# Kernel optimization log

Hardware: AMD Instinct MI355X
Metric: run time of the kernel (lower is better)

The kernel has to match this reference:

```python
import jax, jax.numpy as jnp
import numpy as np

N, E = 50000, 800000
IN, MID, OUT = 128, 256, 128
LN_EPS = 1e-5


def layer_norm(x, gamma, beta, eps=LN_EPS):
    mu = jnp.mean(x, axis=-1, keepdims=True)
    var = jnp.mean(jnp.square(x - mu), axis=-1, keepdims=True)
    return (x - mu) * jax.lax.rsqrt(var + eps) * gamma + beta


def gcn_conv(x, W, b, src, dst, norm, n):
    # x' = D^{-1/2}(A+I)D^{-1/2} X W + b  (self-loops already folded into src/dst/norm)
    h = x @ W                                  # [N, F_out]
    msg = h[src] * norm[:, None]               # [E+N, F_out] gather + scale
    out = jax.ops.segment_sum(msg, dst, num_segments=n)
    return out + b


def setup_inputs() -> dict:
    key = jax.random.key(0)
    ks = jax.random.split(key, 4)
    x = jax.random.normal(ks[0], (N, IN), dtype=jnp.float32)
    edge_index = jax.random.randint(ks[1], (2, E), 0, N, dtype=jnp.int32)
    W1 = jax.random.normal(ks[2], (IN, MID), dtype=jnp.float32) * (1.0 / np.sqrt(IN))
    b1 = jnp.zeros((MID,), jnp.float32)
    g1 = jnp.ones((IN,), jnp.float32)
    be1 = jnp.zeros((IN,), jnp.float32)
    W4 = jax.random.normal(ks[3], (MID, OUT), dtype=jnp.float32) * (1.0 / np.sqrt(MID))
    b4 = jnp.zeros((OUT,), jnp.float32)
    g4 = jnp.ones((MID,), jnp.float32)
    be4 = jnp.zeros((MID,), jnp.float32)
    return {"x": x, "W1": W1, "b1": b1, "g1": g1, "be1": be1,
            "W4": W4, "b4": b4, "g4": g4, "be4": be4,
            "edge_index": edge_index}


def reference(x, W1, b1, g1, be1, W4, b4, g4, be4, edge_index):
    n = x.shape[0]
    loop = jnp.arange(n, dtype=edge_index.dtype)
    src = jnp.concatenate([edge_index[0], loop])   # [E+N]
    dst = jnp.concatenate([edge_index[1], loop])   # [E+N]
    deg = jax.ops.segment_sum(jnp.ones_like(src, x.dtype), dst, num_segments=n)
    dinv = jax.lax.rsqrt(deg)                      # deg >= 1 thanks to self-loops
    norm = dinv[src] * dinv[dst]                   # [E+N]

    h = gcn_conv(layer_norm(x, g1, be1), W1, b1, src, dst, norm, n)
    h = jax.nn.gelu(h, approximate=False)          # torch F.gelu default = exact erf
    h = gcn_conv(layer_norm(h, g4, be4), W4, b4, src, dst, norm, n)
    return h
```

## Files before the change

### kernel.cpp

```cpp
#include <hip/hip_runtime.h>
#include <math.h>

#define N_NODES 50000
#define E_EDGES 800000

typedef __attribute__((ext_vector_type(4))) float f32x4;
typedef __attribute__((ext_vector_type(8))) short s16x8;

#define T1_OFF    0UL
#define A1H_OFF   12800000UL
#define A1L_OFF   25600000UL
#define T2B_OFF   38400000UL
#define WB1H_OFF  64000000UL
#define WB1L_OFF  64100096UL
#define WB4H_OFF  64200192UL
#define WB4L_OFF  64300288UL
#define DINV_OFF  64400384UL
#define HIST8_OFF 64600384UL
#define RP8_OFF   66200384UL
#define POSREL_OFF 67800448UL
#define CSRS_OFF  71000448UL
#define BSUM_OFF  74200448UL

__device__ __forceinline__ float lo16f(unsigned u) { return __uint_as_float(u << 16); }
__device__ __forceinline__ float hi16f(unsigned u) { return __uint_as_float(u & 0xffff0000u); }
__device__ __forceinline__ unsigned pack2bf(float a, float b) {
  unsigned ua = __float_as_uint(a); ua += 0x7fffu + ((ua >> 16) & 1u);
  unsigned ub = __float_as_uint(b); ub += 0x7fffu + ((ub >> 16) & 1u);
  return (ua >> 16) | (ub & 0xffff0000u);
}
__device__ __forceinline__ float gelu_f(float x) {
  return 0.5f * x * (1.f + erff(x * 0.70710678118654752f));
}

__device__ __forceinline__ void convW_body(const float* __restrict__ W,
                                           unsigned* __restrict__ Wh,
                                           unsigned* __restrict__ Wl,
                                           int K, int N, int tid) {
  if (tid >= (K * N) / 8) return;
  int c15 = tid & 15;
  int kg  = (tid >> 4) & 3;
  int KS  = K >> 5;
  int ks  = (tid >> 6) % KS;
  int nt  = (tid >> 6) / KS;
  int col = nt * 16 + c15;
  int k0  = ks * 32 + kg * 8;
  float w[8];
  #pragma unroll
  for (int j = 0; j < 8; ++j) w[j] = W[(size_t)(k0 + j) * N + col];
  uint4 h, l;
  h.x = pack2bf(w[0], w[1]); l.x = pack2bf(w[0] - lo16f(h.x), w[1] - hi16f(h.x));
  h.y = pack2bf(w[2], w[3]); l.y = pack2bf(w[2] - lo16f(h.y), w[3] - hi16f(h.y));
  h.z = pack2bf(w[4], w[5]); l.z = pack2bf(w[4] - lo16f(h.z), w[5] - hi16f(h.z));
  h.w = pack2bf(w[6], w[7]); l.w = pack2bf(w[6] - lo16f(h.w), w[7] - hi16f(h.w));
  *reinterpret_cast<uint4*>(Wh + (size_t)tid * 4) = h;
  *reinterpret_cast<uint4*>(Wl + (size_t)tid * 4) = l;
}

__global__ __launch_bounds__(256) void prep_kernel(const float* __restrict__ x,
                                                   const float* __restrict__ g,
                                                   const float* __restrict__ be,
                                                   unsigned* __restrict__ T,
                                                   const float* __restrict__ W1,
                                                   const float* __restrict__ W4,
                                                   unsigned* __restrict__ Wh1,
                                                   unsigned* __restrict__ Wl1,
                                                   unsigned* __restrict__ Wh4,
                                                   unsigned* __restrict__ Wl4,
                                                   int4* __restrict__ hist8v) {
  int b = blockIdx.x;
  if (b < 12500) {
    int lane = threadIdx.x & 63, wv = threadIdx.x >> 6;
    int row = b * 4 + wv;
    float2 v = *reinterpret_cast<const float2*>(x + (size_t)row * 128 + lane * 2);
    float s = v.x + v.y, sq = v.x * v.x + v.y * v.y;
    #pragma unroll
    for (int m = 1; m < 64; m <<= 1) { s += __shfl_xor(s, m); sq += __shfl_xor(sq, m); }
    float mu = s * (1.f / 128.f);
    float var = sq * (1.f / 128.f) - mu * mu;
    float rs = rsqrtf(var + 1e-5f);
    float2 gg = *reinterpret_cast<const float2*>(g + lane * 2);
    float2 bb = *reinterpret_cast<const float2*>(be + lane * 2);
    T[(size_t)row * 64 + lane] =
        pack2bf((v.x - mu) * rs * gg.x + bb.x, (v.y - mu) * rs * gg.y + bb.y);
  } else if (b < 12891) {
    int i = (b - 12500) * 256 + threadIdx.x;
    if (i < 100000) hist8v[i] = make_int4(0, 0, 0, 0);
  } else {
    int bb = b - 12891;
    if (bb < 16) convW_body(W1, Wh1, Wl1, 128, 256, bb * 256 + threadIdx.x);
    else         convW_body(W4, Wh4, Wl4, 256, 128, (bb - 16) * 256 + threadIdx.x);
  }
}

__global__ __launch_bounds__(256) void edge_pos(const int* __restrict__ dst,
                                                int* __restrict__ hist8,
                                                unsigned short* __restrict__ posrel) {
  int t4 = blockIdx.x * 256 + threadIdx.x;
  if (t4 >= E_EDGES / 4) return;
  int e = t4 * 4;
  int seg = blockIdx.x & 7;
  int4 d = *reinterpret_cast<const int4*>(dst + e);
  unsigned long long r = 0;
  r |= (unsigned long long)(unsigned short)atomicAdd(&hist8[d.x * 8 + seg], 1);
  r |= (unsigned long long)(unsigned short)atomicAdd(&hist8[d.y * 8 + seg], 1) << 16;
  r |= (unsigned long long)(unsigned short)atomicAdd(&hist8[d.z * 8 + seg], 1) << 32;
  r |= (unsigned long long)(unsigned short)atomicAdd(&hist8[d.w * 8 + seg], 1) << 48;
  __builtin_nontemporal_store(r, reinterpret_cast<unsigned long long*>(posrel + e));
}

__global__ __launch_bounds__(1024) void scan_partial(const int* __restrict__ hist,
                                                     int* __restrict__ rp,
                                                     int* __restrict__ bsum,
                                                     float* __restrict__ dinv, int n) {
  __shared__ int wsum[16];
  int tid = threadIdx.x, lane = tid & 63, wv = tid >> 6;
  int i = blockIdx.x * 1024 + tid;
  int v = (i < n) ? hist[i] : 0;
  int s8 = v;
  #pragma unroll
  for (int m = 1; m < 8; m <<= 1) s8 += __shfl_xor(s8, m);
  if ((i & 7) == 0 && i < n) dinv[i >> 3] = rsqrtf((float)(s8 + 1));
  int sc = v;
  #pragma unroll
  for (int m = 1; m < 64; m <<= 1) { int o = __shfl_up(sc, m); if (lane >= m) sc += o; }
  if (lane == 63) wsum[wv] = sc;
  __syncthreads();
  if (wv == 0) {
    int w = (lane < 16) ? wsum[lane] : 0;
    int swc = w;
    #pragma unroll
    for (int m = 1; m < 16; m <<= 1) { int o = __shfl_up(swc, m); if (lane >= m) swc += o; }
    if (lane < 16) wsum[lane] = swc - w;
    if (lane == 15) bsum[blockIdx.x] = swc;
  }
  __syncthreads();
  if (i < n) rp[i] = (sc - v) + wsum[wv];
}

__global__ __launch_bounds__(64) void scan_bsums(int* __restrict__ bsum, int nb) {
  int lane = threadIdx.x;
  int carry = 0;
  for (int base = 0; base < nb; base += 64) {
    int i = base + lane;
    int v = (i < nb) ? bsum[i] : 0;
    int sc = v;
    #pragma unroll
    for (int m = 1; m < 64; m <<= 1) { int o = __shfl_up(sc, m); if (lane >= m) sc += o; }
    if (i < nb) bsum[i] = carry + sc - v;
    carry += __shfl(sc, 63);
  }
  if (lane == 0) bsum[nb] = carry;
}

__global__ __launch_bounds__(1024) void scan_add(int* __restrict__ rp,
                                                 const int* __restrict__ bsum, int n) {
  int i = blockIdx.x * 1024 + threadIdx.x;
  if (i < n) rp[i] += bsum[blockIdx.x];
  if (i == 0) rp[n] = bsum[gridDim.x];
}

__global__ __launch_bounds__(256) void fill2(const int* __restrict__ src,
                                             const int* __restrict__ dst,
                                             const int* __restrict__ rp8,
                                             const unsigned short* __restrict__ posrel,
                                             unsigned short* __restrict__ csr_src) {
  int t4 = blockIdx.x * 256 + threadIdx.x;
  if (t4 >= E_EDGES / 4) return;
  int e = t4 * 4;
  int seg = blockIdx.x & 7;
  int4 s = *reinterpret_cast<const int4*>(src + e);
  int4 d = *reinterpret_cast<const int4*>(dst + e);
  unsigned long long pr =
      *reinterpret_cast<const unsigned long long*>(posrel + e);
  __builtin_nontemporal_store((unsigned short)s.x,
      csr_src + rp8[d.x * 8 + seg] + (int)(pr & 0xffff));
  __builtin_nontemporal_store((unsigned short)s.y,
      csr_src + rp8[d.y * 8 + seg] + (int)((pr >> 16) & 0xffff));
  __builtin_nontemporal_store((unsigned short)s.z,
      csr_src + rp8[d.z * 8 + seg] + (int)((pr >> 32) & 0xffff));
  __builtin_nontemporal_store((unsigned short)s.w,
      csr_src + rp8[d.w * 8 + seg] + (int)((pr >> 48) & 0xffff));
}

template <int MODE>
__global__ __launch_bounds__(256) void agg128(const unsigned* __restrict__ T,
                                              const int* __restrict__ rp8,
                                              const unsigned short* __restrict__ csr,
                                              const float* __restrict__ dinv,
                                              const float* __restrict__ b,
                                              float* __restrict__ out,
                                              unsigned* __restrict__ outh,
                                              unsigned* __restrict__ outl) {
  int lane = threadIdx.x & 63, wv = threadIdx.x >> 6;
  int node = blockIdx.x * 4 + wv;
  float di = dinv[node], sn = di * di;
  unsigned us = T[(size_t)node * 64 + lane];
  float a0 = lo16f(us) * sn, a1 = hi16f(us) * sn;
  float b0 = 0.f, b1 = 0.f;
  int e = rp8[node * 8], e1 = rp8[node * 8 + 8];
  if (e + 7 < e1) {
    int sA[8];
    #pragma unroll
    for (int j = 0; j < 8; ++j) sA[j] = csr[e + j];
    for (;;) {
      unsigned u[8];
      float nn[8];
      #pragma unroll
      for (int j = 0; j < 8; ++j) u[j] = T[(size_t)sA[j] * 64 + lane];
      #pragma unroll
      for (int j = 0; j < 8; ++j) nn[j] = dinv[sA[j]];
      e += 8;
      bool more = (e + 7 < e1);
      int sB[8];
      if (more) {
        #pragma unroll
        for (int j = 0; j < 8; ++j) sB[j] = csr[e + j];
      }
      #pragma unroll
      for (int j = 0; j < 8; ++j) {
        float nr = nn[j] * di;
        if (j & 1) { b0 += lo16f(u[j]) * nr; b1 += hi16f(u[j]) * nr; }
        else       { a0 += lo16f(u[j]) * nr; a1 += hi16f(u[j]) * nr; }
      }
      if (!more) break;
      #pragma unroll
      for (int j = 0; j < 8; ++j) sA[j] = sB[j];
    }
  }
  for (; e < e1; ++e) {
    int s = csr[e];
    unsigned u = T[(size_t)s * 64 + lane];
    float nr = dinv[s] * di;
    a0 += lo16f(u) * nr; a1 += hi16f(u) * nr;
  }
  a0 += b0; a1 += b1;
  if (MODE == 0) {
    unsigned h = pack2bf(a0, a1);
    float r0 = a0 - lo16f(h), r1 = a1 - hi16f(h);
    outh[(size_t)node * 64 + lane] = h;
    outl[(size_t)node * 64 + lane] = pack2bf(r0, r1);
  } else {
    float2 bb = *reinterpret_cast<const float2*>(b + lane * 2);
    *reinterpret_cast<float2*>(out + (size_t)node * 128 + lane * 2) =
        make_float2(a0 + bb.x, a1 + bb.y);
  }
}

__global__ __launch_bounds__(256) void gemm1_fused(const unsigned* __restrict__ Ah,
                                                   const unsigned* __restrict__ Al,
                                                   const unsigned* __restrict__ Wh,
                                                   const unsigned* __restrict__ Wl,
                                                   const float* __restrict__ b,
                                                   const float* __restrict__ g,
                                                   const float* __restrict__ be,
                                                   unsigned* __restrict__ T2b, int n) {
  __shared__ float st[32 * 260];
  int t = threadIdx.x, lane = t & 63, w = t >> 6;
  int kg = lane >> 4, c15 = lane & 15;
  int c0 = w * 64;
  int row0 = blockIdx.x * 32 + c15;
  int r0 = min(row0, n - 1);
  int r1 = min(row0 + 16, n - 1);
  const unsigned* ah0 = Ah + (size_t)r0 * 64 + kg * 4;
  const unsigned* al0 = Al + (size_t)r0 * 64 + kg * 4;
  const unsigned* ah1 = Ah + (size_t)r1 * 64 + kg * 4;
  const unsigned* al1 = Al + (size_t)r1 * 64 + kg * 4;
  f32x4 acc[2][4];
  #pragma unroll
  for (int rt = 0; rt < 2; ++rt)
    #pragma unroll
    for (int nf = 0; nf < 4; ++nf) acc[rt][nf] = (f32x4)(0.f);
  #pragma unroll
  for (int ks = 0; ks < 4; ++ks) {
    s16x8 bh[4], bl[4];
    #pragma unroll
    for (int nf = 0; nf < 4; ++nf) {
      int nt = (c0 >> 4) + nf;
      size_t bo = (size_t)(((nt * 4 + ks) * 4 + kg) * 16 + c15) * 4;
      bh[nf] = *reinterpret_cast<const s16x8*>(Wh + bo);
      bl[nf] = *reinterpret_cast<const s16x8*>(Wl + bo);
    }
    s16x8 a0h = *reinterpret_cast<const s16x8*>(ah0 + ks * 16);
    s16x8 a0l = *reinterpret_cast<const s16x8*>(al0 + ks * 16);
    s16x8 a1h = *reinterpret_cast<const s16x8*>(ah1 + ks * 16);
    s16x8 a1l = *reinterpret_cast<const s16x8*>(al1 + ks * 16);
    #pragma unroll
    for (int nf = 0; nf < 4; ++nf) {
      acc[0][nf] = __builtin_amdgcn_mfma_f32_16x16x32_bf16(a0h, bh[nf], acc[0][nf], 0, 0, 0);
      acc[0][nf] = __builtin_amdgcn_mfma_f32_16x16x32_bf16(a0l, bh[nf], acc[0][nf], 0, 0, 0);
      acc[0][nf] = __builtin_amdgcn_mfma_f32_16x16x32_bf16(a0h, bl[nf], acc[0][nf], 0, 0, 0);
      acc[1][nf] = __builtin_amdgcn_mfma_f32_16x16x32_bf16(a1h, bh[nf], acc[1][nf], 0, 0, 0);
      acc[1][nf] = __builtin_amdgcn_mfma_f32_16x16x32_bf16(a1l, bh[nf], acc[1][nf], 0, 0, 0);
      acc[1][nf] = __builtin_amdgcn_mfma_f32_16x16x32_bf16(a1h, bl[nf], acc[1][nf], 0, 0, 0);
    }
  }
  #pragma unroll
  for (int rt = 0; rt < 2; ++rt)
    #pragma unroll
    for (int nf = 0; nf < 4; ++nf) {
      int col = c0 + nf * 16 + c15;
      float bb = b[col];
      #pragma unroll
      for (int r = 0; r < 4; ++r) {
        int row = rt * 16 + kg * 4 + r;
        st[row * 260 + col] = gelu_f(acc[rt][nf][r] + bb);
      }
    }
  __syncthreads();
  float4 gg = *reinterpret_cast<const float4*>(g + lane * 4);
  float4 bb2 = *reinterpret_cast<const float4*>(be + lane * 4);
  #pragma unroll
  for (int rr = 0; rr < 8; ++rr) {
    int row = w * 8 + rr;
    float4 v = *reinterpret_cast<const float4*>(&st[row * 260 + lane * 4]);
    float s = v.x + v.y + v.z + v.w;
    float sq = v.x * v.x + v.y * v.y + v.z * v.z + v.w * v.w;
    #pragma unroll
    for (int m = 1; m < 64; m <<= 1) { s += __shfl_xor(s, m); sq += __shfl_xor(sq, m); }
    float mu = s * (1.f / 256.f);
    float var = sq * (1.f / 256.f) - mu * mu;
    float rs = rsqrtf(var + 1e-5f);
    int gr = blockIdx.x * 32 + row;
    if (gr < n) {
      uint2 p;
      p.x = pack2bf((v.x - mu) * rs * gg.x + bb2.x, (v.y - mu) * rs * gg.y + bb2.y);
      p.y = pack2bf((v.z - mu) * rs * gg.z + bb2.z, (v.w - mu) * rs * gg.w + bb2.w);
      *reinterpret_cast<uint2*>(T2b + (size_t)gr * 128 + lane * 2) = p;
    }
  }
}

__global__ __launch_bounds__(256) void gemm2_mfma(const unsigned* __restrict__ Ab,
                                                  const unsigned* __restrict__ Wh,
                                                  const unsigned* __restrict__ Wl,
                                                  unsigned* __restrict__ T2, int n) {
  __shared__ float st[32 * 132];
  int t = threadIdx.x, lane = t & 63, w = t >> 6;
  int kg = lane >> 4, c15 = lane & 15;
  int c0 = w * 32;
  int row0 = blockIdx.x * 32 + c15;
  int r0 = min(row0, n - 1);
  int r1 = min(row0 + 16, n - 1);
  const unsigned* ap0 = Ab + (size_t)r0 * 128 + kg * 4;
  const unsigned* ap1 = Ab + (size_t)r1 * 128 + kg * 4;
  f32x4 acc[2][2];
  #pragma unroll
  for (int rt = 0; rt < 2; ++rt) { acc[rt][0] = (f32x4)(0.f); acc[rt][1] = (f32x4)(0.f); }
  #pragma unroll
  for (int ks = 0; ks < 8; ++ks) {
    s16x8 bh[2], bl[2];
    #pragma unroll
    for (int nf = 0; nf < 2; ++nf) {
      int nt = (c0 >> 4) + nf;
      size_t bo = (size_t)(((nt * 8 + ks) * 4 + kg) * 16 + c15) * 4;
      bh[nf] = *reinterpret_cast<const s16x8*>(Wh + bo);
      bl[nf] = *reinterpret_cast<const s16x8*>(Wl + bo);
    }
    s16x8 a0 = *reinterpret_cast<const s16x8*>(ap0 + ks * 16);
    s16x8 a1 = *reinterpret_cast<const s16x8*>(ap1 + ks * 16);
    #pragma unroll
    for (int nf = 0; nf < 2; ++nf) {
      acc[0][nf] = __builtin_amdgcn_mfma_f32_16x16x32_bf16(a0, bh[nf], acc[0][nf], 0, 0, 0);
      acc[0][nf] = __builtin_amdgcn_mfma_f32_16x16x32_bf16(a0, bl[nf], acc[0][nf], 0, 0, 0);
      acc[1][nf] = __builtin_amdgcn_mfma_f32_16x16x32_bf16(a1, bh[nf], acc[1][nf], 0, 0, 0);
      acc[1][nf] = __builtin_amdgcn_mfma_f32_16x16x32_bf16(a1, bl[nf], acc[1][nf], 0, 0, 0);
    }
  }
  #pragma unroll
  for (int rt = 0; rt < 2; ++rt)
    #pragma unroll
    for (int nf = 0; nf < 2; ++nf) {
      int col = c0 + nf * 16 + c15;
      #pragma unroll
      for (int r = 0; r < 4; ++r) {
        int row = rt * 16 + kg * 4 + r;
        st[row * 132 + col] = acc[rt][nf][r];
      }
    }
  __syncthreads();
  #pragma unroll
  for (int rr = 0; rr < 8; ++rr) {
    int row = w * 8 + rr;
    int gr = blockIdx.x * 32 + row;
    if (gr < n) {
      float2 v = *reinterpret_cast<const float2*>(&st[row * 132 + lane * 2]);
      T2[(size_t)gr * 64 + lane] = pack2bf(v.x, v.y);
    }
  }
}

extern "C" void kernel_launch(void* const* d_in, const int* in_sizes, int n_in,
                              void* d_out, int out_size, void* d_ws, size_t ws_size,
                              hipStream_t stream) {
  (void)in_sizes; (void)n_in; (void)out_size; (void)ws_size;
  const float* x   = (const float*)d_in[0];
  const float* W1  = (const float*)d_in[1];
  const float* b1  = (const float*)d_in[2];
  const float* g1  = (const float*)d_in[3];
  const float* be1 = (const float*)d_in[4];
  const float* W4  = (const float*)d_in[5];
  const float* b4  = (const float*)d_in[6];
  const float* g4  = (const float*)d_in[7];
  const float* be4 = (const float*)d_in[8];
  const int*   ei  = (const int*)d_in[9];
  const int* src = ei;
  const int* dst = ei + E_EDGES;

  char* ws = (char*)d_ws;
  unsigned* T1    = (unsigned*)(ws + T1_OFF);
  unsigned* T2    = (unsigned*)(ws + T1_OFF);
  unsigned* A1h   = (unsigned*)(ws + A1H_OFF);
  unsigned* A1l   = (unsigned*)(ws + A1L_OFF);
  unsigned* T2b   = (unsigned*)(ws + T2B_OFF);
  unsigned* Wb1h  = (unsigned*)(ws + WB1H_OFF);
  unsigned* Wb1l  = (unsigned*)(ws + WB1L_OFF);
  unsigned* Wb4h  = (unsigned*)(ws + WB4H_OFF);
  unsigned* Wb4l  = (unsigned*)(ws + WB4L_OFF);
  float* dinv     = (float*)(ws + DINV_OFF);
  int*   hist8    = (int*)(ws + HIST8_OFF);
  int*   rp8      = (int*)(ws + RP8_OFF);
  unsigned short* posrel  = (unsigned short*)(ws + POSREL_OFF);
  unsigned short* csr_src = (unsigned short*)(ws + CSRS_OFF);
  int*   bsum     = (int*)(ws + BSUM_OFF);
  float* outp     = (float*)d_out;

  const int NSEG = N_NODES * 8;
  int nblkE4 = (E_EDGES / 4 + 255) / 256;
  int nbScan = (NSEG + 1023) / 1024;
  int nblkG  = (N_NODES + 31) / 32;
  int nblkP  = 12500 + 391 + 32;

  hipLaunchKernelGGL(prep_kernel, dim3(nblkP), dim3(256), 0, stream,
                     x, g1, be1, T1, W1, W4, Wb1h, Wb1l, Wb4h, Wb4l, (int4*)hist8);
  hipLaunchKernelGGL(edge_pos, dim3(nblkE4), dim3(256), 0, stream, dst, hist8, posrel);
  hipLaunchKernelGGL(scan_partial, dim3(nbScan), dim3(1024), 0, stream,
                     hist8, rp8, bsum, dinv, NSEG);
  hipLaunchKernelGGL(scan_bsums, dim3(1), dim3(64), 0, stream, bsum, nbScan);
  hipLaunchKernelGGL(scan_add, dim3(nbScan), dim3(1024), 0, stream, rp8, bsum, NSEG);
  hipLaunchKernelGGL(fill2, dim3(nblkE4), dim3(256), 0, stream, src, dst, rp8, posrel, csr_src);

  hipLaunchKernelGGL(agg128<0>, dim3(N_NODES / 4), dim3(256), 0, stream,
                     T1, rp8, csr_src, dinv, (const float*)nullptr,
                     (float*)nullptr, A1h, A1l);
  hipLaunchKernelGGL(gemm1_fused, dim3(nblkG), dim3(256), 0, stream,
                     A1h, A1l, Wb1h, Wb1l, b1, g4, be4, T2b, N_NODES);

  hipLaunchKernelGGL(gemm2_mfma, dim3(nblkG), dim3(256), 0, stream, T2b, Wb4h, Wb4l, T2, N_NODES);
  hipLaunchKernelGGL(agg128<2>, dim3(N_NODES / 4), dim3(256), 0, stream,
                     T2, rp8, csr_src, dinv, b4, outp,
                     (unsigned*)nullptr, (unsigned*)nullptr);
}
```

Before: 230.7 us.

## Chunk feature tables into 32-column slabs and precompute fp16 edge norms in CSR

Feature tables T1/T2 are stored as four column chunks (16 dwords per node each), so each aggregation block handles one chunk for a group of nodes. The goal is a smaller per-chunk working set that stays in cache during the random gathers. The CSR entries now pack the source index with a precomputed fp16 normalization, removing the per-edge dinv gathers. Each wavefront processes four edges in parallel and reduces across quarter-wavefronts with shuffles. The cost is eight times as many aggregation blocks, a 32-bit CSR that is twice the size, and fp16 rounding of the norm coefficients.

New measurement: 271.2 us. 1.18x slower.

```diff
diff --git a/kernel.cpp b/kernel.cpp
--- a/kernel.cpp
+++ b/kernel.cpp
@@ -1,8 +1,10 @@
 #include <hip/hip_runtime.h>
+#include <hip/hip_fp16.h>
 #include <math.h>
 
 #define N_NODES 50000
 #define E_EDGES 800000
+#define CHUNK_U (N_NODES * 16)
 
 typedef __attribute__((ext_vector_type(4))) float f32x4;
 typedef __attribute__((ext_vector_type(8))) short s16x8;
@@ -19,7 +21,7 @@
 #define HIST8_OFF 64600384UL
 #define RP8_OFF   66200384UL
 #define POSREL_OFF 67800448UL
-#define CSRS_OFF  71000448UL
+#define CSR_OFF   71000448UL
 #define BSUM_OFF  74200448UL
 
 __device__ __forceinline__ float lo16f(unsigned u) { return __uint_as_float(u << 16); }
@@ -31,6 +33,14 @@
 }
 __device__ __forceinline__ float gelu_f(float x) {
   return 0.5f * x * (1.f + erff(x * 0.70710678118654752f));
+}
+__device__ __forceinline__ unsigned short f2h_bits(float f) {
+  __half h = __float2half_rn(f);
+  return *reinterpret_cast<unsigned short*>(&h);
+}
+__device__ __forceinline__ float h_bits2f(unsigned short u) {
+  __half h = *reinterpret_cast<__half*>(&u);
+  return __half2float(h);
 }
 
 __device__ __forceinline__ void convW_body(const float* __restrict__ W,
@@ -81,7 +91,7 @@
     float rs = rsqrtf(var + 1e-5f);
     float2 gg = *reinterpret_cast<const float2*>(g + lane * 2);
     float2 bb = *reinterpret_cast<const float2*>(be + lane * 2);
-    T[(size_t)row * 64 + lane] =
+    T[(size_t)(lane >> 4) * CHUNK_U + (size_t)row * 16 + (lane & 15)] =
         pack2bf((v.x - mu) * rs * gg.x + bb.x, (v.y - mu) * rs * gg.y + bb.y);
   } else if (b < 12891) {
     int i = (b - 12500) * 256 + threadIdx.x;
@@ -164,86 +174,91 @@
                                              const int* __restrict__ dst,
                                              const int* __restrict__ rp8,
                                              const unsigned short* __restrict__ posrel,
-                                             unsigned short* __restrict__ csr_src) {
+                                             const float* __restrict__ dinv,
+                                             unsigned* __restrict__ csr) {
   int t4 = blockIdx.x * 256 + threadIdx.x;
   if (t4 >= E_EDGES / 4) return;
   int e = t4 * 4;
   int seg = blockIdx.x & 7;
   int4 s = *reinterpret_cast<const int4*>(src + e);
   int4 d = *reinterpret_cast<const int4*>(dst + e);
-  unsigned long long pr =
-      *reinterpret_cast<const unsigned long long*>(posrel + e);
-  __builtin_nontemporal_store((unsigned short)s.x,
-      csr_src + rp8[d.x * 8 + seg] + (int)(pr & 0xffff));
-  __builtin_nontemporal_store((unsigned short)s.y,
-      csr_src + rp8[d.y * 8 + seg] + (int)((pr >> 16) & 0xffff));
-  __builtin_nontemporal_store((unsigned short)s.z,
-      csr_src + rp8[d.z * 8 + seg] + (int)((pr >> 32) & 0xffff));
-  __builtin_nontemporal_store((unsigned short)s.w,
-      csr_src + rp8[d.w * 8 + seg] + (int)((pr >> 48) & 0xffff));
+  unsigned long long pr = *reinterpret_cast<const unsigned long long*>(posrel + e);
+  int ss[4] = {s.x, s.y, s.z, s.w};
+  int dd[4] = {d.x, d.y, d.z, d.w};
+  #pragma unroll
+  for (int j = 0; j < 4; ++j) {
+    int pos = rp8[dd[j] * 8 + seg] + (int)((pr >> (16 * j)) & 0xffff);
+    float nr = dinv[ss[j]] * dinv[dd[j]];
+    unsigned pk = ((unsigned)f2h_bits(nr) << 16) | (unsigned)ss[j];
+    __builtin_nontemporal_store(pk, csr + pos);
+  }
 }
 
 template <int MODE>
-__global__ __launch_bounds__(256) void agg128(const unsigned* __restrict__ T,
-                                              const int* __restrict__ rp8,
-                                              const unsigned short* __restrict__ csr,
-                                              const float* __restrict__ dinv,
-                                              const float* __restrict__ b,
-                                              float* __restrict__ out,
-                                              unsigned* __restrict__ outh,
-                                              unsigned* __restrict__ outl) {
-  int lane = threadIdx.x & 63, wv = threadIdx.x >> 6;
-  int node = blockIdx.x * 4 + wv;
-  float di = dinv[node], sn = di * di;
-  unsigned us = T[(size_t)node * 64 + lane];
-  float a0 = lo16f(us) * sn, a1 = hi16f(us) * sn;
+__global__ __launch_bounds__(256) void agg32(const unsigned* __restrict__ Tc,
+                                             const int* __restrict__ rp8,
+                                             const unsigned* __restrict__ csr,
+                                             const float* __restrict__ dinv,
+                                             const float* __restrict__ b,
+                                             float* __restrict__ out,
+                                             unsigned* __restrict__ outh,
+                                             unsigned* __restrict__ outl) {
+  int t = threadIdx.x, lane = t & 63, wv = t >> 6;
+  int bid = blockIdx.x;
+  int cid = bid & 7;
+  int chunk = cid >> 1, half = cid & 1;
+  int node = (bid >> 3) * 8 + half * 4 + wv;
+  int q = lane >> 4, l16 = lane & 15;
+  const unsigned* Tch = Tc + (size_t)chunk * CHUNK_U;
+  float a0 = 0.f, a1 = 0.f;
   float b0 = 0.f, b1 = 0.f;
-  int e = rp8[node * 8], e1 = rp8[node * 8 + 8];
-  if (e + 7 < e1) {
-    int sA[8];
-    #pragma unroll
-    for (int j = 0; j < 8; ++j) sA[j] = csr[e + j];
-    for (;;) {
-      unsigned u[8];
-      float nn[8];
-      #pragma unroll
-      for (int j = 0; j < 8; ++j) u[j] = T[(size_t)sA[j] * 64 + lane];
-      #pragma unroll
-      for (int j = 0; j < 8; ++j) nn[j] = dinv[sA[j]];
-      e += 8;
-      bool more = (e + 7 < e1);
-      int sB[8];
-      if (more) {
-        #pragma unroll
-        for (int j = 0; j < 8; ++j) sB[j] = csr[e + j];
-      }
-      #pragma unroll
-      for (int j = 0; j < 8; ++j) {
-        float nr = nn[j] * di;
-        if (j & 1) { b0 += lo16f(u[j]) * nr; b1 += hi16f(u[j]) * nr; }
-        else       { a0 += lo16f(u[j]) * nr; a1 += hi16f(u[j]) * nr; }
-      }
-      if (!more) break;
-      #pragma unroll
-      for (int j = 0; j < 8; ++j) sA[j] = sB[j];
-    }
-  }
-  for (; e < e1; ++e) {
-    int s = csr[e];
-    unsigned u = T[(size_t)s * 64 + lane];
-    float nr = dinv[s] * di;
-    a0 += lo16f(u) * nr; a1 += hi16f(u) * nr;
+  int e0 = rp8[node * 8], e1 = rp8[node * 8 + 8];
+  int e = e0;
+  for (; e + 16 <= e1; e += 16) {
+    unsigned c0 = csr[e + q];
+    unsigned c1 = csr[e + 4 + q];
+    unsigned c2 = csr[e + 8 + q];
+    unsigned c3 = csr[e + 12 + q];
+    unsigned u0 = Tch[(size_t)(c0 & 0xffffu) * 16 + l16];
+    unsigned u1 = Tch[(size_t)(c1 & 0xffffu) * 16 + l16];
+    unsigned u2 = Tch[(size_t)(c2 & 0xffffu) * 16 + l16];
+    unsigned u3 = Tch[(size_t)(c3 & 0xffffu) * 16 + l16];
+    float n0 = h_bits2f((unsigned short)(c0 >> 16));
+    float n1 = h_bits2f((unsigned short)(c1 >> 16));
+    float n2 = h_bits2f((unsigned short)(c2 >> 16));
+    float n3 = h_bits2f((unsigned short)(c3 >> 16));
+    a0 += lo16f(u0) * n0; a1 += hi16f(u0) * n0;
+    b0 += lo16f(u1) * n1; b1 += hi16f(u1) * n1;
+    a0 += lo16f(u2) * n2; a1 += hi16f(u2) * n2;
+    b0 += lo16f(u3) * n3; b1 += hi16f(u3) * n3;
+  }
+  if (e < e1) {
+    #pragma unroll
+    for (int j = 0; j < 4; ++j) {
+      int idx = e + j * 4 + q;
+      bool valid = idx < e1;
+      unsigned c = csr[valid ? idx : e0];
+      unsigned u = Tch[(size_t)(c & 0xffffu) * 16 + l16];
+      float nr = valid ? h_bits2f((unsigned short)(c >> 16)) : 0.f;
+      a0 += lo16f(u) * nr; a1 += hi16f(u) * nr;
+    }
   }
   a0 += b0; a1 += b1;
-  if (MODE == 0) {
-    unsigned h = pack2bf(a0, a1);
-    float r0 = a0 - lo16f(h), r1 = a1 - hi16f(h);
-    outh[(size_t)node * 64 + lane] = h;
-    outl[(size_t)node * 64 + lane] = pack2bf(r0, r1);
-  } else {
-    float2 bb = *reinterpret_cast<const float2*>(b + lane * 2);
-    *reinterpret_cast<float2*>(out + (size_t)node * 128 + lane * 2) =
-        make_float2(a0 + bb.x, a1 + bb.y);
+  a0 += __shfl_xor(a0, 16); a1 += __shfl_xor(a1, 16);
+  a0 += __shfl_xor(a0, 32); a1 += __shfl_xor(a1, 32);
+  if (q == 0) {
+    float di = dinv[node], sn = di * di;
+    unsigned us = Tch[(size_t)node * 16 + l16];
+    a0 += lo16f(us) * sn; a1 += hi16f(us) * sn;
+    if (MODE == 0) {
+      unsigned h = pack2bf(a0, a1);
+      outh[(size_t)node * 64 + chunk * 16 + l16] = h;
+      outl[(size_t)node * 64 + chunk * 16 + l16] = pack2bf(a0 - lo16f(h), a1 - hi16f(h));
+    } else {
+      float2 bb = *reinterpret_cast<const float2*>(b + chunk * 32 + l16 * 2);
+      *reinterpret_cast<float2*>(out + (size_t)node * 128 + chunk * 32 + l16 * 2) =
+          make_float2(a0 + bb.x, a1 + bb.y);
+    }
   }
 }
 
@@ -385,7 +400,7 @@
     int gr = blockIdx.x * 32 + row;
     if (gr < n) {
       float2 v = *reinterpret_cast<const float2*>(&st[row * 132 + lane * 2]);
-      T2[(size_t)gr * 64 + lane] = pack2bf(v.x, v.y);
+      T2[(size_t)(lane >> 4) * CHUNK_U + (size_t)gr * 16 + (lane & 15)] = pack2bf(v.x, v.y);
     }
   }
 }
@@ -420,8 +435,8 @@
   float* dinv     = (float*)(ws + DINV_OFF);
   int*   hist8    = (int*)(ws + HIST8_OFF);
   int*   rp8      = (int*)(ws + RP8_OFF);
-  unsigned short* posrel  = (unsigned short*)(ws + POSREL_OFF);
-  unsigned short* csr_src = (unsigned short*)(ws + CSRS_OFF);
+  unsigned short* posrel = (unsigned short*)(ws + POSREL_OFF);
+  unsigned* csr   = (unsigned*)(ws + CSR_OFF);
   int*   bsum     = (int*)(ws + BSUM_OFF);
   float* outp     = (float*)d_out;
 
@@ -430,6 +445,7 @@
   int nbScan = (NSEG + 1023) / 1024;
   int nblkG  = (N_NODES + 31) / 32;
   int nblkP  = 12500 + 391 + 32;
+  int nblkA  = (N_NODES / 8) * 8;
 
   hipLaunchKernelGGL(prep_kernel, dim3(nblkP), dim3(256), 0, stream,
                      x, g1, be1, T1, W1, W4, Wb1h, Wb1l, Wb4h, Wb4l, (int4*)hist8);
@@ -438,16 +454,17 @@
                      hist8, rp8, bsum, dinv, NSEG);
   hipLaunchKernelGGL(scan_bsums, dim3(1), dim3(64), 0, stream, bsum, nbScan);
   hipLaunchKernelGGL(scan_add, dim3(nbScan), dim3(1024), 0, stream, rp8, bsum, NSEG);
-  hipLaunchKernelGGL(fill2, dim3(nblkE4), dim3(256), 0, stream, src, dst, rp8, posrel, csr_src);
-
-  hipLaunchKernelGGL(agg128<0>, dim3(N_NODES / 4), dim3(256), 0, stream,
-                     T1, rp8, csr_src, dinv, (const float*)nullptr,
+  hipLaunchKernelGGL(fill2, dim3(nblkE4), dim3(256), 0, stream,
+                     src, dst, rp8, posrel, dinv, csr);
+
+  hipLaunchKernelGGL(agg32<0>, dim3(nblkA), dim3(256), 0, stream,
+                     T1, rp8, csr, dinv, (const float*)nullptr,
                      (float*)nullptr, A1h, A1l);
   hipLaunchKernelGGL(gemm1_fused, dim3(nblkG), dim3(256), 0, stream,
                      A1h, A1l, Wb1h, Wb1l, b1, g4, be4, T2b, N_NODES);
 
   hipLaunchKernelGGL(gemm2_mfma, dim3(nblkG), dim3(256), 0, stream, T2b, Wb4h, Wb4l, T2, N_NODES);
-  hipLaunchKernelGGL(agg128<2>, dim3(N_NODES / 4), dim3(256), 0, stream,
-                     T2, rp8, csr_src, dinv, b4, outp,
+  hipLaunchKernelGGL(agg32<2>, dim3(nblkA), dim3(256), 0, stream,
+                     T2, rp8, csr, dinv, b4, outp,
                      (unsigned*)nullptr, (unsigned*)nullptr);
 }
```

## Fuse layer-1 aggregation into GEMM1 kernel via shared-memory tiles

Applied to the files above, without the earlier changes.

Merges the first-layer neighbour aggregation with the following GEMM+bias+GELU+LayerNorm kernel. Each block aggregates its 32 nodes into LDS as bf16 hi/lo splits and feeds MFMA directly, so the 128-wide A1 hi/lo intermediates no longer round-trip through global memory and one launch disappears. The LayerNorm epilogue also changes from an LDS-staged full row to register-resident values with a cross-wave reduction through small LDS arrays, then writes bf16 per element. The cost is that each block now serialises 8 node aggregations per wave before its GEMM, and the grid has far fewer blocks, which may reduce latency hiding for the gather-bound part.

After: 268.0 us. 1.16x slower.

```diff
diff --git a/kernel.cpp b/kernel.cpp
--- a/kernel.cpp
+++ b/kernel.cpp
@@ -8,8 +8,6 @@
 typedef __attribute__((ext_vector_type(8))) short s16x8;
 
 #define T1_OFF    0UL
-#define A1H_OFF   12800000UL
-#define A1L_OFF   25600000UL
 #define T2B_OFF   38400000UL
 #define WB1H_OFF  64000000UL
 #define WB1L_OFF  64100096UL
@@ -28,6 +26,10 @@
   unsigned ua = __float_as_uint(a); ua += 0x7fffu + ((ua >> 16) & 1u);
   unsigned ub = __float_as_uint(b); ub += 0x7fffu + ((ub >> 16) & 1u);
   return (ua >> 16) | (ub & 0xffff0000u);
+}
+__device__ __forceinline__ unsigned short bf16r(float f) {
+  unsigned ua = __float_as_uint(f); ua += 0x7fffu + ((ua >> 16) & 1u);
+  return (unsigned short)(ua >> 16);
 }
 __device__ __forceinline__ float gelu_f(float x) {
   return 0.5f * x * (1.f + erff(x * 0.70710678118654752f));
@@ -171,8 +173,7 @@
   int seg = blockIdx.x & 7;
   int4 s = *reinterpret_cast<const int4*>(src + e);
   int4 d = *reinterpret_cast<const int4*>(dst + e);
-  unsigned long long pr =
-      *reinterpret_cast<const unsigned long long*>(posrel + e);
+  unsigned long long pr = *reinterpret_cast<const unsigned long long*>(posrel + e);
   __builtin_nontemporal_store((unsigned short)s.x,
       csr_src + rp8[d.x * 8 + seg] + (int)(pr & 0xffff));
   __builtin_nontemporal_store((unsigned short)s.y,
@@ -183,89 +184,77 @@
       csr_src + rp8[d.w * 8 + seg] + (int)((pr >> 48) & 0xffff));
 }
 
-template <int MODE>
-__global__ __launch_bounds__(256) void agg128(const unsigned* __restrict__ T,
-                                              const int* __restrict__ rp8,
-                                              const unsigned short* __restrict__ csr,
-                                              const float* __restrict__ dinv,
-                                              const float* __restrict__ b,
-                                              float* __restrict__ out,
-                                              unsigned* __restrict__ outh,
-                                              unsigned* __restrict__ outl) {
-  int lane = threadIdx.x & 63, wv = threadIdx.x >> 6;
-  int node = blockIdx.x * 4 + wv;
-  float di = dinv[node], sn = di * di;
-  unsigned us = T[(size_t)node * 64 + lane];
-  float a0 = lo16f(us) * sn, a1 = hi16f(us) * sn;
-  float b0 = 0.f, b1 = 0.f;
-  int e = rp8[node * 8], e1 = rp8[node * 8 + 8];
-  if (e + 7 < e1) {
-    int sA[8];
-    #pragma unroll
-    for (int j = 0; j < 8; ++j) sA[j] = csr[e + j];
-    for (;;) {
-      unsigned u[8];
-      float nn[8];
-      #pragma unroll
-      for (int j = 0; j < 8; ++j) u[j] = T[(size_t)sA[j] * 64 + lane];
-      #pragma unroll
-      for (int j = 0; j < 8; ++j) nn[j] = dinv[sA[j]];
-      e += 8;
-      bool more = (e + 7 < e1);
-      int sB[8];
-      if (more) {
+__global__ __launch_bounds__(256) void layer1_fused(
+    const unsigned* __restrict__ T,
+    const int* __restrict__ rp8,
+    const unsigned short* __restrict__ csr,
+    const float* __restrict__ dinv,
+    const unsigned* __restrict__ Wh,
+    const unsigned* __restrict__ Wl,
+    const float* __restrict__ b,
+    const float* __restrict__ g,
+    const float* __restrict__ be,
+    unsigned short* __restrict__ T2b,
+    int n) {
+  __shared__ unsigned AhL[32][68];
+  __shared__ unsigned AlL[32][68];
+  __shared__ float rsum[32][4];
+  __shared__ float rsq[32][4];
+  int t = threadIdx.x, lane = t & 63, w = t >> 6;
+
+  for (int i = 0; i < 8; ++i) {
+    int nl = w * 8 + i;
+    int node = blockIdx.x * 32 + nl;
+    if (node >= n) node = n - 1;
+    float di = dinv[node], sn = di * di;
+    unsigned us = T[(size_t)node * 64 + lane];
+    float a0 = lo16f(us) * sn, a1 = hi16f(us) * sn;
+    float b0 = 0.f, b1_ = 0.f;
+    int e = rp8[node * 8], e1 = rp8[node * 8 + 8];
+    if (e + 7 < e1) {
+      int sA[8];
+      #pragma unroll
+      for (int j = 0; j < 8; ++j) sA[j] = csr[e + j];
+      for (;;) {
+        unsigned u[8];
+        float nn[8];
         #pragma unroll
-        for (int j = 0; j < 8; ++j) sB[j] = csr[e + j];
+        for (int j = 0; j < 8; ++j) u[j] = T[(size_t)sA[j] * 64 + lane];
+        #pragma unroll
+        for (int j = 0; j < 8; ++j) nn[j] = dinv[sA[j]];
+        e += 8;
+        bool more = (e + 7 < e1);
+        int sB[8];
+        if (more) {
+          #pragma unroll
+          for (int j = 0; j < 8; ++j) sB[j] = csr[e + j];
+        }
+        #pragma unroll
+        for (int j = 0; j < 8; ++j) {
+          float nr = nn[j] * di;
+          if (j & 1) { b0 += lo16f(u[j]) * nr; b1_ += hi16f(u[j]) * nr; }
+          else       { a0 += lo16f(u[j]) * nr; a1 += hi16f(u[j]) * nr; }
+        }
+        if (!more) break;
+        #pragma unroll
+        for (int j = 0; j < 8; ++j) sA[j] = sB[j];
       }
-      #pragma unroll
-      for (int j = 0; j < 8; ++j) {
-        float nr = nn[j] * di;
-        if (j & 1) { b0 += lo16f(u[j]) * nr; b1 += hi16f(u[j]) * nr; }
-        else       { a0 += lo16f(u[j]) * nr; a1 += hi16f(u[j]) * nr; }
-      }
-      if (!more) break;
-      #pragma unroll
-      for (int j = 0; j < 8; ++j) sA[j] = sB[j];
-    }
-  }
-  for (; e < e1; ++e) {
-    int s = csr[e];
-    unsigned u = T[(size_t)s * 64 + lane];
-    float nr = dinv[s] * di;
-    a0 += lo16f(u) * nr; a1 += hi16f(u) * nr;
-  }
-  a0 += b0; a1 += b1;
-  if (MODE == 0) {
+    }
+    for (; e < e1; ++e) {
+      int s = csr[e];
+      unsigned u = T[(size_t)s * 64 + lane];
+      float nr = dinv[s] * di;
+      a0 += lo16f(u) * nr; a1 += hi16f(u) * nr;
+    }
+    a0 += b0; a1 += b1_;
     unsigned h = pack2bf(a0, a1);
-    float r0 = a0 - lo16f(h), r1 = a1 - hi16f(h);
-    outh[(size_t)node * 64 + lane] = h;
-    outl[(size_t)node * 64 + lane] = pack2bf(r0, r1);
-  } else {
-    float2 bb = *reinterpret_cast<const float2*>(b + lane * 2);
-    *reinterpret_cast<float2*>(out + (size_t)node * 128 + lane * 2) =
-        make_float2(a0 + bb.x, a1 + bb.y);
-  }
-}
-
-__global__ __launch_bounds__(256) void gemm1_fused(const unsigned* __restrict__ Ah,
-                                                   const unsigned* __restrict__ Al,
-                                                   const unsigned* __restrict__ Wh,
-                                                   const unsigned* __restrict__ Wl,
-                                                   const float* __restrict__ b,
-                                                   const float* __restrict__ g,
-                                                   const float* __restrict__ be,
-                                                   unsigned* __restrict__ T2b, int n) {
-  __shared__ float st[32 * 260];
-  int t = threadIdx.x, lane = t & 63, w = t >> 6;
+    AhL[nl][lane] = h;
+    AlL[nl][lane] = pack2bf(a0 - lo16f(h), a1 - hi16f(h));
+  }
+  __syncthreads();
+
   int kg = lane >> 4, c15 = lane & 15;
   int c0 = w * 64;
-  int row0 = blockIdx.x * 32 + c15;
-  int r0 = min(row0, n - 1);
-  int r1 = min(row0 + 16, n - 1);
-  const unsigned* ah0 = Ah + (size_t)r0 * 64 + kg * 4;
-  const unsigned* al0 = Al + (size_t)r0 * 64 + kg * 4;
-  const unsigned* ah1 = Ah + (size_t)r1 * 64 + kg * 4;
-  const unsigned* al1 = Al + (size_t)r1 * 64 + kg * 4;
   f32x4 acc[2][4];
   #pragma unroll
   for (int rt = 0; rt < 2; ++rt)
@@ -281,10 +270,10 @@
       bh[nf] = *reinterpret_cast<const s16x8*>(Wh + bo);
       bl[nf] = *reinterpret_cast<const s16x8*>(Wl + bo);
     }
-    s16x8 a0h = *reinterpret_cast<const s16x8*>(ah0 + ks * 16);
-    s16x8 a0l = *reinterpret_cast<const s16x8*>(al0 + ks * 16);
-    s16x8 a1h = *reinterpret_cast<const s16x8*>(ah1 + ks * 16);
-    s16x8 a1l = *reinterpret_cast<const s16x8*>(al1 + ks * 16);
+    s16x8 a0h = *reinterpret_cast<const s16x8*>(&AhL[c15][kg * 4 + ks * 16]);
+    s16x8 a0l = *reinterpret_cast<const s16x8*>(&AlL[c15][kg * 4 + ks * 16]);
+    s16x8 a1h = *reinterpret_cast<const s16x8*>(&AhL[16 + c15][kg * 4 + ks * 16]);
+    s16x8 a1l = *reinterpret_cast<const s16x8*>(&AlL[16 + c15][kg * 4 + ks * 16]);
     #pragma unroll
     for (int nf = 0; nf < 4; ++nf) {
       acc[0][nf] = __builtin_amdgcn_mfma_f32_16x16x32_bf16(a0h, bh[nf], acc[0][nf], 0, 0, 0);
@@ -295,40 +284,57 @@
       acc[1][nf] = __builtin_amdgcn_mfma_f32_16x16x32_bf16(a1h, bl[nf], acc[1][nf], 0, 0, 0);
     }
   }
+
+  float hv[2][4][4];
+  float bb[4], gg[4], be2[4];
+  #pragma unroll
+  for (int nf = 0; nf < 4; ++nf) {
+    int col = c0 + nf * 16 + c15;
+    bb[nf] = b[col]; gg[nf] = g[col]; be2[nf] = be[col];
+  }
   #pragma unroll
   for (int rt = 0; rt < 2; ++rt)
     #pragma unroll
-    for (int nf = 0; nf < 4; ++nf) {
-      int col = c0 + nf * 16 + c15;
-      float bb = b[col];
-      #pragma unroll
-      for (int r = 0; r < 4; ++r) {
+    for (int nf = 0; nf < 4; ++nf)
+      #pragma unroll
+      for (int r = 0; r < 4; ++r)
+        hv[rt][nf][r] = gelu_f(acc[rt][nf][r] + bb[nf]);
+
+  #pragma unroll
+  for (int rt = 0; rt < 2; ++rt)
+    #pragma unroll
+    for (int r = 0; r < 4; ++r) {
+      float s = hv[rt][0][r] + hv[rt][1][r] + hv[rt][2][r] + hv[rt][3][r];
+      float q = hv[rt][0][r] * hv[rt][0][r] + hv[rt][1][r] * hv[rt][1][r] +
+                hv[rt][2][r] * hv[rt][2][r] + hv[rt][3][r] * hv[rt][3][r];
+      #pragma unroll
+      for (int m = 1; m < 16; m <<= 1) { s += __shfl_xor(s, m); q += __shfl_xor(q, m); }
+      if (c15 == 0) {
         int row = rt * 16 + kg * 4 + r;
-        st[row * 260 + col] = gelu_f(acc[rt][nf][r] + bb);
+        rsum[row][w] = s; rsq[row][w] = q;
       }
     }
   __syncthreads();
-  float4 gg = *reinterpret_cast<const float4*>(g + lane * 4);
-  float4 bb2 = *reinterpret_cast<const float4*>(be + lane * 4);
-  #pragma unroll
-  for (int rr = 0; rr < 8; ++rr) {
-    int row = w * 8 + rr;
-    float4 v = *reinterpret_cast<const float4*>(&st[row * 260 + lane * 4]);
-    float s = v.x + v.y + v.z + v.w;
-    float sq = v.x * v.x + v.y * v.y + v.z * v.z + v.w * v.w;
-    #pragma unroll
-    for (int m = 1; m < 64; m <<= 1) { s += __shfl_xor(s, m); sq += __shfl_xor(sq, m); }
-    float mu = s * (1.f / 256.f);
-    float var = sq * (1.f / 256.f) - mu * mu;
-    float rs = rsqrtf(var + 1e-5f);
-    int gr = blockIdx.x * 32 + row;
-    if (gr < n) {
-      uint2 p;
-      p.x = pack2bf((v.x - mu) * rs * gg.x + bb2.x, (v.y - mu) * rs * gg.y + bb2.y);
-      p.y = pack2bf((v.z - mu) * rs * gg.z + bb2.z, (v.w - mu) * rs * gg.w + bb2.w);
-      *reinterpret_cast<uint2*>(T2b + (size_t)gr * 128 + lane * 2) = p;
-    }
-  }
+  #pragma unroll
+  for (int rt = 0; rt < 2; ++rt)
+    #pragma unroll
+    for (int r = 0; r < 4; ++r) {
+      int row = rt * 16 + kg * 4 + r;
+      float S = rsum[row][0] + rsum[row][1] + rsum[row][2] + rsum[row][3];
+      float Q = rsq[row][0] + rsq[row][1] + rsq[row][2] + rsq[row][3];
+      float mu = S * (1.f / 256.f);
+      float var = Q * (1.f / 256.f) - mu * mu;
+      float rs = rsqrtf(var + 1e-5f);
+      int gr = blockIdx.x * 32 + row;
+      if (gr < n) {
+        #pragma unroll
+        for (int nf = 0; nf < 4; ++nf) {
+          int col = c0 + nf * 16 + c15;
+          float o = (hv[rt][nf][r] - mu) * rs * gg[nf] + be2[nf];
+          T2b[(size_t)gr * 256 + col] = bf16r(o);
+        }
+      }
+    }
 }
 
 __global__ __launch_bounds__(256) void gemm2_mfma(const unsigned* __restrict__ Ab,
@@ -388,6 +394,60 @@
       T2[(size_t)gr * 64 + lane] = pack2bf(v.x, v.y);
     }
   }
+}
+
+__global__ __launch_bounds__(256) void agg128_final(const unsigned* __restrict__ T,
+                                                    const int* __restrict__ rp8,
+                                                    const unsigned short* __restrict__ csr,
+                                                    const float* __restrict__ dinv,
+                                                    const float* __restrict__ b,
+                                                    float* __restrict__ out) {
+  int lane = threadIdx.x & 63, wv = threadIdx.x >> 6;
+  int node = blockIdx.x * 4 + wv;
+  float di = dinv[node], sn = di * di;
+  unsigned us = T[(size_t)node * 64 + lane];
+  float a0 = lo16f(us) * sn, a1 = hi16f(us) * sn;
+  float b0 = 0.f, b1 = 0.f;
+  int e = rp8[node * 8], e1 = rp8[node * 8 + 8];
+  if (e + 7 < e1) {
+    int sA[8];
+    #pragma unroll
+    for (int j = 0; j < 8; ++j) sA[j] = csr[e + j];
+    for (;;) {
+      unsigned u[8];
+      float nn[8];
+      #pragma unroll
+      for (int j = 0; j < 8; ++j) u[j] = T[(size_t)sA[j] * 64 + lane];
+      #pragma unroll
+      for (int j = 0; j < 8; ++j) nn[j] = dinv[sA[j]];
+      e += 8;
+      bool more = (e + 7 < e1);
+      int sB[8];
+      if (more) {
+        #pragma unroll
+        for (int j = 0; j < 8; ++j) sB[j] = csr[e + j];
+      }
+      #pragma unroll
+      for (int j = 0; j < 8; ++j) {
+        float nr = nn[j] * di;
+        if (j & 1) { b0 += lo16f(u[j]) * nr; b1 += hi16f(u[j]) * nr; }
+        else       { a0 += lo16f(u[j]) * nr; a1 += hi16f(u[j]) * nr; }
+      }
+      if (!more) break;
+      #pragma unroll
+      for (int j = 0; j < 8; ++j) sA[j] = sB[j];
+    }
+  }
+  for (; e < e1; ++e) {
+    int s = csr[e];
+    unsigned u = T[(size_t)s * 64 + lane];
+    float nr = dinv[s] * di;
+    a0 += lo16f(u) * nr; a1 += hi16f(u) * nr;
+  }
+  a0 += b0; a1 += b1;
+  float2 bb = *reinterpret_cast<const float2*>(b + lane * 2);
+  *reinterpret_cast<float2*>(out + (size_t)node * 128 + lane * 2) =
+      make_float2(a0 + bb.x, a1 + bb.y);
 }
 
 extern "C" void kernel_launch(void* const* d_in, const int* in_sizes, int n_in,
@@ -410,9 +470,7 @@
   char* ws = (char*)d_ws;
   unsigned* T1    = (unsigned*)(ws + T1_OFF);
   unsigned* T2    = (unsigned*)(ws + T1_OFF);
-  unsigned* A1h   = (unsigned*)(ws + A1H_OFF);
-  unsigned* A1l   = (unsigned*)(ws + A1L_OFF);
-  unsigned* T2b   = (unsigned*)(ws + T2B_OFF);
+  unsigned short* T2b = (unsigned short*)(ws + T2B_OFF);
   unsigned* Wb1h  = (unsigned*)(ws + WB1H_OFF);
   unsigned* Wb1l  = (unsigned*)(ws + WB1L_OFF);
   unsigned* Wb4h  = (unsigned*)(ws + WB4H_OFF);
@@ -440,14 +498,11 @@
   hipLaunchKernelGGL(scan_add, dim3(nbScan), dim3(1024), 0, stream, rp8, bsum, NSEG);
   hipLaunchKernelGGL(fill2, dim3(nblkE4), dim3(256), 0, stream, src, dst, rp8, posrel, csr_src);
 
-  hipLaunchKernelGGL(agg128<0>, dim3(N_NODES / 4), dim3(256), 0, stream,
-                     T1, rp8, csr_src, dinv, (const float*)nullptr,
-                     (float*)nullptr, A1h, A1l);
-  hipLaunchKernelGGL(gemm1_fused, dim3(nblkG), dim3(256), 0, stream,
-                     A1h, A1l, Wb1h, Wb1l, b1, g4, be4, T2b, N_NODES);
-
-  hipLaunchKernelGGL(gemm2_mfma, dim3(nblkG), dim3(256), 0, stream, T2b, Wb4h, Wb4l, T2, N_NODES);
-  hipLaunchKernelGGL(agg128<2>, dim3(N_NODES / 4), dim3(256), 0, stream,
-                     T2, rp8, csr_src, dinv, b4, outp,
-                     (unsigned*)nullptr, (unsigned*)nullptr);
-}
+  hipLaunchKernelGGL(layer1_fused, dim3(nblkG), dim3(256), 0, stream,
+                     T1, rp8, csr_src, dinv, Wb1h, Wb1l, b1, g4, be4, T2b, N_NODES);
+
+  hipLaunchKernelGGL(gemm2_mfma, dim3(nblkG), dim3(256), 0, stream,
+                     (const unsigned*)T2b, Wb4h, Wb4l, T2, N_NODES);
+  hipLaunchKernelGGL(agg128_final, dim3(N_NODES / 4), dim3(256), 0, stream,
+                     T2, rp8, csr_src, dinv, b4, outp);
+}
```

## Drop low-order bf16 split of aggregated activations and fold block-sum scan into scan_add

Applied to the files above, without the earlier changes.

The first aggregation now writes only a single bf16 copy of its result instead of a hi/lo bf16 pair. The first GEMM therefore skips the residual A-operand loads and two of its six MFMAs per tile. Separately, the single-wave block-sum scan kernel is removed: each scan_add block rescans the small bsum array in its first wave to find its own offset, saving one launch. The cost is reduced precision in the first GEMM input, since the residual correction term is lost, plus a small amount of redundant scan work per block.

Measured after the change: 223.5 us. 1.03x faster.

```diff
diff --git a/kernel.cpp b/kernel.cpp
--- a/kernel.cpp
+++ b/kernel.cpp
@@ -9,7 +9,6 @@
 
 #define T1_OFF    0UL
 #define A1H_OFF   12800000UL
-#define A1L_OFF   25600000UL
 #define T2B_OFF   38400000UL
 #define WB1H_OFF  64000000UL
 #define WB1L_OFF  64100096UL
@@ -138,26 +137,28 @@
   if (i < n) rp[i] = (sc - v) + wsum[wv];
 }
 
-__global__ __launch_bounds__(64) void scan_bsums(int* __restrict__ bsum, int nb) {
-  int lane = threadIdx.x;
-  int carry = 0;
-  for (int base = 0; base < nb; base += 64) {
-    int i = base + lane;
-    int v = (i < nb) ? bsum[i] : 0;
-    int sc = v;
-    #pragma unroll
-    for (int m = 1; m < 64; m <<= 1) { int o = __shfl_up(sc, m); if (lane >= m) sc += o; }
-    if (i < nb) bsum[i] = carry + sc - v;
-    carry += __shfl(sc, 63);
-  }
-  if (lane == 0) bsum[nb] = carry;
-}
-
 __global__ __launch_bounds__(1024) void scan_add(int* __restrict__ rp,
-                                                 const int* __restrict__ bsum, int n) {
-  int i = blockIdx.x * 1024 + threadIdx.x;
-  if (i < n) rp[i] += bsum[blockIdx.x];
-  if (i == 0) rp[n] = bsum[gridDim.x];
+                                                 const int* __restrict__ bsum,
+                                                 int n, int nb) {
+  __shared__ int off_s, tot_s;
+  int tid = threadIdx.x;
+  if (tid < 64) {
+    int carry = 0;
+    for (int base = 0; base < nb; base += 64) {
+      int i = base + tid;
+      int v = (i < nb) ? bsum[i] : 0;
+      int sc = v;
+      #pragma unroll
+      for (int m = 1; m < 64; m <<= 1) { int o = __shfl_up(sc, m); if (tid >= m) sc += o; }
+      if (i == (int)blockIdx.x) off_s = carry + sc - v;
+      carry += __shfl(sc, 63);
+    }
+    if (tid == 0) tot_s = carry;
+  }
+  __syncthreads();
+  int i = blockIdx.x * 1024 + tid;
+  if (i < n) rp[i] += off_s;
+  if (i == 0) rp[n] = tot_s;
 }
 
 __global__ __launch_bounds__(256) void fill2(const int* __restrict__ src,
@@ -171,8 +172,7 @@
   int seg = blockIdx.x & 7;
   int4 s = *reinterpret_cast<const int4*>(src + e);
   int4 d = *reinterpret_cast<const int4*>(dst + e);
-  unsigned long long pr =
-      *reinterpret_cast<const unsigned long long*>(posrel + e);
+  unsigned long long pr = *reinterpret_cast<const unsigned long long*>(posrel + e);
   __builtin_nontemporal_store((unsigned short)s.x,
       csr_src + rp8[d.x * 8 + seg] + (int)(pr & 0xffff));
   __builtin_nontemporal_store((unsigned short)s.y,
@@ -190,8 +190,7 @@
                                               const float* __restrict__ dinv,
                                               const float* __restrict__ b,
                                               float* __restrict__ out,
-                                              unsigned* __restrict__ outh,
-                                              unsigned* __restrict__ outl) {
+                                              unsigned* __restrict__ outh) {
   int lane = threadIdx.x & 63, wv = threadIdx.x >> 6;
   int node = blockIdx.x * 4 + wv;
   float di = dinv[node], sn = di * di;
@@ -236,10 +235,7 @@
   }
   a0 += b0; a1 += b1;
   if (MODE == 0) {
-    unsigned h = pack2bf(a0, a1);
-    float r0 = a0 - lo16f(h), r1 = a1 - hi16f(h);
-    outh[(size_t)node * 64 + lane] = h;
-    outl[(size_t)node * 64 + lane] = pack2bf(r0, r1);
+    outh[(size_t)node * 64 + lane] = pack2bf(a0, a1);
   } else {
     float2 bb = *reinterpret_cast<const float2*>(b + lane * 2);
     *reinterpret_cast<float2*>(out + (size_t)node * 128 + lane * 2) =
@@ -248,7 +244,6 @@
 }
 
 __global__ __launch_bounds__(256) void gemm1_fused(const unsigned* __restrict__ Ah,
-                                                   const unsigned* __restrict__ Al,
                                                    const unsigned* __restrict__ Wh,
                                                    const unsigned* __restrict__ Wl,
                                                    const float* __restrict__ b,
@@ -263,9 +258,7 @@
   int r0 = min(row0, n - 1);
   int r1 = min(row0 + 16, n - 1);
   const unsigned* ah0 = Ah + (size_t)r0 * 64 + kg * 4;
-  const unsigned* al0 = Al + (size_t)r0 * 64 + kg * 4;
   const unsigned* ah1 = Ah + (size_t)r1 * 64 + kg * 4;
-  const unsigned* al1 = Al + (size_t)r1 * 64 + kg * 4;
   f32x4 acc[2][4];
   #pragma unroll
   for (int rt = 0; rt < 2; ++rt)
@@ -282,16 +275,12 @@
       bl[nf] = *reinterpret_cast<const s16x8*>(Wl + bo);
     }
     s16x8 a0h = *reinterpret_cast<const s16x8*>(ah0 + ks * 16);
-    s16x8 a0l = *reinterpret_cast<const s16x8*>(al0 + ks * 16);
     s16x8 a1h = *reinterpret_cast<const s16x8*>(ah1 + ks * 16);
-    s16x8 a1l = *reinterpret_cast<const s16x8*>(al1 + ks * 16);
     #pragma unroll
     for (int nf = 0; nf < 4; ++nf) {
       acc[0][nf] = __builtin_amdgcn_mfma_f32_16x16x32_bf16(a0h, bh[nf], acc[0][nf], 0, 0, 0);
-      acc[0][nf] = __builtin_amdgcn_mfma_f32_16x16x32_bf16(a0l, bh[nf], acc[0][nf], 0, 0, 0);
       acc[0][nf] = __builtin_amdgcn_mfma_f32_16x16x32_bf16(a0h, bl[nf], acc[0][nf], 0, 0, 0);
       acc[1][nf] = __builtin_amdgcn_mfma_f32_16x16x32_bf16(a1h, bh[nf], acc[1][nf], 0, 0, 0);
-      acc[1][nf] = __builtin_amdgcn_mfma_f32_16x16x32_bf16(a1l, bh[nf], acc[1][nf], 0, 0, 0);
       acc[1][nf] = __builtin_amdgcn_mfma_f32_16x16x32_bf16(a1h, bl[nf], acc[1][nf], 0, 0, 0);
     }
   }
@@ -411,7 +400,6 @@
   unsigned* T1    = (unsigned*)(ws + T1_OFF);
   unsigned* T2    = (unsigned*)(ws + T1_OFF);
   unsigned* A1h   = (unsigned*)(ws + A1H_OFF);
-  unsigned* A1l   = (unsigned*)(ws + A1L_OFF);
   unsigned* T2b   = (unsigned*)(ws + T2B_OFF);
   unsigned* Wb1h  = (unsigned*)(ws + WB1H_OFF);
   unsigned* Wb1l  = (unsigned*)(ws + WB1L_OFF);
@@ -436,18 +424,16 @@
   hipLaunchKernelGGL(edge_pos, dim3(nblkE4), dim3(256), 0, stream, dst, hist8, posrel);
   hipLaunchKernelGGL(scan_partial, dim3(nbScan), dim3(1024), 0, stream,
                      hist8, rp8, bsum, dinv, NSEG);
-  hipLaunchKernelGGL(scan_bsums, dim3(1), dim3(64), 0, stream, bsum, nbScan);
-  hipLaunchKernelGGL(scan_add, dim3(nbScan), dim3(1024), 0, stream, rp8, bsum, NSEG);
+  hipLaunchKernelGGL(scan_add, dim3(nbScan), dim3(1024), 0, stream, rp8, bsum, NSEG, nbScan);
   hipLaunchKernelGGL(fill2, dim3(nblkE4), dim3(256), 0, stream, src, dst, rp8, posrel, csr_src);
 
   hipLaunchKernelGGL(agg128<0>, dim3(N_NODES / 4), dim3(256), 0, stream,
                      T1, rp8, csr_src, dinv, (const float*)nullptr,
-                     (float*)nullptr, A1h, A1l);
+                     (float*)nullptr, A1h);
   hipLaunchKernelGGL(gemm1_fused, dim3(nblkG), dim3(256), 0, stream,
-                     A1h, A1l, Wb1h, Wb1l, b1, g4, be4, T2b, N_NODES);
+                     A1h, Wb1h, Wb1l, b1, g4, be4, T2b, N_NODES);
 
   hipLaunchKernelGGL(gemm2_mfma, dim3(nblkG), dim3(256), 0, stream, T2b, Wb4h, Wb4l, T2, N_NODES);
   hipLaunchKernelGGL(agg128<2>, dim3(N_NODES / 4), dim3(256), 0, stream,
-                     T2, rp8, csr_src, dinv, b4, outp,
-                     (unsigned*)nullptr, (unsigned*)nullptr);
-}
+                     T2, rp8, csr_src, dinv, b4, outp, (unsigned*)nullptr);
+}
```
